# Optimization experiments

Measured on AMD Instinct MI355X. Metric: run time of the kernel, lower is better.

Reference implementation:

```python
import jax, jax.numpy as jnp
import numpy as np

BATCH, SEQ, DIM = 4, 4096, 256
DT_RANK, D_STATE, NUM_TOKENS = 16, 16, 1024


def _adapool(x, T):
    # uniform window mean == AdaptiveAvgPool1d when S % T == 0
    B, S, D = x.shape
    return x.reshape(B, T, S // T, D).mean(axis=2)


def _layernorm(x, g, b, eps=1e-5):
    mu = x.mean(-1, keepdims=True)
    var = ((x - mu) ** 2).mean(-1, keepdims=True)
    return (x - mu) * jax.lax.rsqrt(var + eps) * g + b


def _gauss_mask(T):
    c = (T + 1) // 2
    idx = jnp.arange(T, dtype=jnp.float32)
    sigma = jnp.abs(idx - c).mean()
    w = jnp.exp(-0.5 * (idx - c) ** 2 / sigma ** 2)
    return w / w.sum()


def _ssm(x, Wdbc, Wdt, bdt, Alog, D):
    A = -jnp.exp(Alog)                                     # (Dm, N)
    dbc = x @ Wdbc.T                                       # (B,L,dt+2N)
    delta = jax.nn.softplus(dbc[..., :DT_RANK] @ Wdt.T + bdt)   # (B,L,Dm)
    Bm = dbc[..., DT_RANK:DT_RANK + D_STATE]               # (B,L,N)
    Cm = dbc[..., DT_RANK + D_STATE:]                      # (B,L,N)
    deltaA = jnp.exp(delta[..., None] * A)                 # (B,L,Dm,N)
    BX = (delta[..., None] * Bm[:, :, None, :]) * x[..., None]
    def comb(c1, c2):
        a1, x1 = c1
        a2, x2 = c2
        return (a2 * a1, a2 * x1 + x2)
    _, hs = jax.lax.associative_scan(comb, (deltaA, BX), axis=1)
    y = jnp.einsum('bldn,bln->bld', hs, Cm) + D * x
    return y


def setup_inputs():
    key = jax.random.key(0)
    ks = jax.random.split(key, 16)
    s = 0.05
    Alog = jnp.tile(jnp.log(jnp.arange(1.0, D_STATE + 1.0, dtype=jnp.float32))[None, :], (DIM, 1))
    return {
        'x': jax.random.normal(ks[0], (BATCH, SEQ, DIM), jnp.float32),
        'ln_g': jnp.ones((DIM,), jnp.float32),
        'ln_b': jnp.zeros((DIM,), jnp.float32),
        'W1': jax.random.normal(ks[1], (DIM, DIM), jnp.float32) * s,
        'b1': jnp.zeros((DIM,), jnp.float32),
        'W2': jax.random.normal(ks[2], (DIM, DIM), jnp.float32) * s,
        'b2': jnp.zeros((DIM,), jnp.float32),
        'Wcf': jax.random.normal(ks[3], (DIM, DIM), jnp.float32) * s,
        'bcf': jnp.zeros((DIM,), jnp.float32),
        'Wcb': jax.random.normal(ks[4], (DIM, DIM), jnp.float32) * s,
        'bcb': jnp.zeros((DIM,), jnp.float32),
        'Wdbc_f': jax.random.normal(ks[5], (DT_RANK + 2 * D_STATE, DIM), jnp.float32) * s,
        'Wdt_f': jax.random.normal(ks[6], (DIM, DT_RANK), jnp.float32) * s,
        'bdt_f': jnp.zeros((DIM,), jnp.float32),
        'Alog_f': Alog,
        'D_f': jnp.ones((DIM,), jnp.float32),
        'Wdbc_b': jax.random.normal(ks[7], (DT_RANK + 2 * D_STATE, DIM), jnp.float32) * s,
        'Wdt_b': jax.random.normal(ks[8], (DIM, DT_RANK), jnp.float32) * s,
        'bdt_b': jnp.zeros((DIM,), jnp.float32),
        'Alog_b': Alog,
        'D_b': jnp.ones((DIM,), jnp.float32),
    }


def reference(x, ln_g, ln_b, W1, b1, W2, b2, Wcf, bcf, Wcb, bcb,
              Wdbc_f, Wdt_f, bdt_f, Alog_f, D_f,
              Wdbc_b, Wdt_b, bdt_b, Alog_b, D_b):
    skip = _adapool(x, NUM_TOKENS)
    xn = _layernorm(x, ln_g, ln_b)
    z = xn @ W1.T + b1
    xp = xn @ W2.T + b2
    mask = _gauss_mask(NUM_TOKENS)[None, :, None]

    # forward direction: 1x1 conv (= channel linear) -> softplus -> SSM
    h1 = jax.nn.softplus(jnp.einsum('bsd,ed->bse', xp, Wcf) + bcf)
    x1 = _ssm(h1, Wdbc_f, Wdt_f, bdt_f, Alog_f, D_f)
    x1 = jax.nn.silu(_adapool(x1, NUM_TOKENS) * mask)

    # backward direction on flipped sequence
    h2 = jax.nn.softplus(jnp.einsum('bsd,ed->bse', xp[:, ::-1], Wcb) + bcb)
    x2 = _ssm(h2, Wdbc_b, Wdt_b, bdt_b, Alog_b, D_b)[:, ::-1]
    x2 = jax.nn.silu(_adapool(x2, NUM_TOKENS) * mask)

    zp = jax.nn.silu(_adapool(z, NUM_TOKENS))
    return zp * x1 + zp * x2 + skip
```

## Files before the change

### kernel.cpp

```cpp
#include <hip/hip_runtime.h>
#include <math.h>


namespace {
constexpr int BB = 4;
constexpr int LL = 4096;
constexpr int DD = 256;
constexpr int NS = 16;
constexpr int NCH = 128;
constexpr int CLEN = 32;
constexpr int NG  = CLEN / 8;
constexpr int TOK = 1024;

constexpr size_t NROW = (size_t)BB * LL;
constexpr size_t NE   = NROW * DD;
constexpr size_t NP   = (size_t)BB * TOK * DD;
constexpr size_t NBC  = NROW * NS;
constexpr size_t NAGG = 2ull * BB * DD * NCH * NS;
constexpr size_t NSD  = 2ull * BB * NCH * DD;

constexpr size_t O_H1X  = 0;
constexpr size_t O_G2X  = NE / 2;
constexpr size_t O_H1T  = NE;
constexpr size_t O_G2T  = NE + NE / 2;
constexpr size_t O_DLTF = 2 * NE;
constexpr size_t O_XN   = O_DLTF;
constexpr size_t O_DLTB = 2 * NE + NE / 2;
constexpr size_t O_BMF  = 3 * NE;
constexpr size_t O_CMF  = O_BMF + NBC / 2;
constexpr size_t O_BMB  = O_CMF + NBC / 2;
constexpr size_t O_CMB  = O_BMB + NBC / 2;
constexpr size_t O_ZP   = O_CMB + NBC / 2;
constexpr size_t O_WF1  = O_ZP + NP;
constexpr size_t O_BF1  = O_WF1 + 768 * 256 / 2;
constexpr size_t O_WF2F = O_BF1 + 768;
constexpr size_t O_B2F  = O_WF2F + 384 * 256 / 2;
constexpr size_t O_WF2B = O_B2F + 384;
constexpr size_t O_B2B  = O_WF2B + 384 * 256 / 2;
constexpr size_t O_SD   = O_B2B + 384;
constexpr size_t O_HEND = O_SD + NSD;
constexpr size_t O_HIN  = O_HEND + NAGG / 2;
constexpr size_t O_MASK = O_HIN + NAGG / 2;

constexpr int SST = 136;
}

typedef __bf16 bf16x8 __attribute__((ext_vector_type(8)));
typedef __bf16 bf16x4 __attribute__((ext_vector_type(4)));
typedef float f32x4 __attribute__((ext_vector_type(4)));

__device__ __forceinline__ float softplusf(float x) {
    return fmaxf(x, 0.f) + __logf(1.f + __expf(-fabsf(x)));
}
__device__ __forceinline__ float siluf(float x) {
    return x / (1.f + __expf(-x));
}
__device__ __forceinline__ void gl_lds16(const void* g, void* l) {
    __builtin_amdgcn_global_load_lds((const __attribute__((address_space(1))) unsigned int*)g,
                                     (__attribute__((address_space(3))) unsigned int*)l, 16, 0, 0);
}
__device__ __forceinline__ int st_addr(int col, int row) {
    return col * SST + ((((row >> 3) ^ (col >> 3)) & 15) << 3) + (row & 7);
}
__device__ __forceinline__ void pow_chain(float e1, float* p) {
    p[0] = e1;
    p[1] = e1 * e1;
    p[2] = p[1] * e1;
    p[3] = p[1] * p[1];
    p[4] = p[3] * p[0];
    p[5] = p[3] * p[1];
    p[6] = p[3] * p[2];
    p[7] = p[3] * p[3];
    p[8]  = p[7] * p[0];
    p[9]  = p[7] * p[1];
    p[10] = p[7] * p[2];
    p[11] = p[7] * p[3];
    p[12] = p[7] * p[4];
    p[13] = p[7] * p[5];
    p[14] = p[7] * p[6];
    p[15] = p[7] * p[7];
}

__global__ __launch_bounds__(256) void prep_ln_kernel(
    const float* __restrict__ x, const float* __restrict__ lng, const float* __restrict__ lnb,
    const float* __restrict__ W1, const float* __restrict__ b1,
    const float* __restrict__ W2, const float* __restrict__ b2,
    const float* __restrict__ Wcf, const float* __restrict__ bcf,
    const float* __restrict__ Wcb, const float* __restrict__ bcb,
    const float* __restrict__ Wdt_f, const float* __restrict__ Wdbc_f, const float* __restrict__ bdt_f,
    const float* __restrict__ Wdt_b, const float* __restrict__ Wdbc_b, const float* __restrict__ bdt_b,
    __bf16* __restrict__ xn, float* __restrict__ outp,
    __bf16* __restrict__ Wf1, float* __restrict__ bf1,
    __bf16* __restrict__ Wf2f, float* __restrict__ b2f,
    __bf16* __restrict__ Wf2b, float* __restrict__ b2b,
    float* __restrict__ mask)
{
    int bxg = blockIdx.x;
    int k = threadIdx.x;
    if (bxg < 4096) {
        __shared__ float red[32];
        __shared__ float mv[8];
        int t = k;
        int r0 = bxg * 4;
        float gg = lng[t], bbv = lnb[t];
        float v[4], s[4], q[4];
#pragma unroll
        for (int i = 0; i < 4; ++i) {
            v[i] = x[(size_t)(r0 + i) * 256 + t];
            s[i] = v[i];
            q[i] = v[i] * v[i];
        }
        for (int o = 32; o > 0; o >>= 1) {
#pragma unroll
            for (int i = 0; i < 4; ++i) {
                s[i] += __shfl_xor(s[i], o, 64);
                q[i] += __shfl_xor(q[i], o, 64);
            }
        }
        if ((t & 63) == 0) {
            int w = t >> 6;
#pragma unroll
            for (int i = 0; i < 4; ++i) { red[i * 4 + w] = s[i]; red[16 + i * 4 + w] = q[i]; }
        }
        __syncthreads();
        if (t < 4) {
            float S = red[t * 4 + 0] + red[t * 4 + 1] + red[t * 4 + 2] + red[t * 4 + 3];
            float Q = red[16 + t * 4 + 0] + red[16 + t * 4 + 1] + red[16 + t * 4 + 2] + red[16 + t * 4 + 3];
            float mu = S * (1.f / 256.f);
            mv[t * 2] = mu;
            mv[t * 2 + 1] = rsqrtf(Q * (1.f / 256.f) - mu * mu + 1e-5f);
        }
        __syncthreads();
        float acc = 0.f;
#pragma unroll
        for (int i = 0; i < 4; ++i) {
            xn[(size_t)(r0 + i) * 256 + t] = (__bf16)((v[i] - mv[i * 2]) * mv[i * 2 + 1] * gg + bbv);
            acc += v[i];
        }
        int b = r0 >> 12;
        int g = (r0 & 4095) >> 2;
        outp[((size_t)b * TOK + g) * 256 + t] = acc * 0.25f;
        return;
    }
    int j2 = bxg - 4096;
    int mat = j2 / 641;
    int bx = j2 % 641;
    if (bx < 256) {
        int j = bx;
        const float* Wc = mat ? Wcb : Wcf;
        float acc = 0.f, accb = 0.f;
#pragma unroll 8
        for (int m = 0; m < 256; ++m) {
            float w = Wc[j * 256 + m];
            acc  = fmaf(w, W2[m * 256 + k], acc);
            accb = fmaf(w, b2[m], accb);
        }
        Wf1[(size_t)(256 + mat * 256 + j) * 256 + k] = (__bf16)acc;
        if (k == 0) bf1[256 + mat * 256 + j] = accb + (mat ? bcb[j] : bcf[j]);
        if (mat == 0) {
            Wf1[(size_t)j * 256 + k] = (__bf16)W1[j * 256 + k];
            if (k == 0) bf1[j] = b1[j];
        }
    } else if (bx < 640) {
        int j = bx - 256;
        const float* Wdt  = mat ? Wdt_b : Wdt_f;
        const float* Wdbc = mat ? Wdbc_b : Wdbc_f;
        const float* bdt  = mat ? bdt_b : bdt_f;
        __bf16* Wf2 = mat ? Wf2b : Wf2f;
        float* b2x  = mat ? b2b : b2f;
        float val;
        if (j < 256) {
            float acc = 0.f;
#pragma unroll
            for (int m = 0; m < 16; ++m)
                acc = fmaf(Wdt[j * 16 + m], Wdbc[m * 256 + k], acc);
            val = acc;
        } else if (j < 288) {
            val = Wdbc[(16 + (j - 256)) * 256 + k];
        } else {
            val = 0.f;
        }
        Wf2[(size_t)j * 256 + k] = (__bf16)val;
        if (k == 0) b2x[j] = (j < 256) ? bdt[j] : 0.f;
    } else if (mat == 0) {
        __shared__ float red2[4];
        __shared__ float sb;
        float w[4];
        float loc = 0.f;
#pragma unroll
        for (int q = 0; q < 4; ++q) {
            float dd = (float)(k + 256 * q) - 512.f;
            w[q] = __expf(-0.5f * dd * dd * (1.f / 65536.f));
            loc += w[q];
        }
        for (int o = 32; o > 0; o >>= 1) loc += __shfl_xor(loc, o, 64);
        if ((k & 63) == 0) red2[k >> 6] = loc;
        __syncthreads();
        if (k == 0) sb = red2[0] + red2[1] + red2[2] + red2[3];
        __syncthreads();
        float inv = 1.f / sb;
#pragma unroll
        for (int q = 0; q < 4; ++q) mask[k + 256 * q] = w[q] * inv;
    }
}

__global__ __launch_bounds__(256) void gemm1_mfma(
    const __bf16* __restrict__ A, const __bf16* __restrict__ Bw, const float* __restrict__ bias,
    float* __restrict__ zp, __bf16* __restrict__ h1x, __bf16* __restrict__ g2x,
    __bf16* __restrict__ h1T, __bf16* __restrict__ g2T)
{
    __shared__ __align__(16) __bf16 SH[128 * SST];
    __bf16* As = SH;
    __bf16* Bs = SH + 8192;
    int tid = threadIdx.x;
    int lane = tid & 63, wv = tid >> 6;
    int wr = wv >> 1, wc = wv & 1;
    int lm = lane & 15, lq = lane >> 4;
    int m0 = blockIdx.x << 7, n0 = blockIdx.y << 7;

    const __bf16* gaB = A  + (size_t)(m0 + wv * 32 + lm) * 256 + lq * 8;
    const __bf16* gbB = Bw + (size_t)(n0 + wv * 32 + lm) * 256 + lq * 8;

    f32x4 acc[4][4];
#pragma unroll
    for (int i = 0; i < 4; ++i)
#pragma unroll
        for (int j = 0; j < 4; ++j) acc[i][j] = 0;

    for (int k0 = 0; k0 < 256; k0 += 64) {
        __syncthreads();
#pragma unroll
        for (int rg = 0; rg < 2; ++rg) {
#pragma unroll
            for (int kh = 0; kh < 2; ++kh) {
                gl_lds16(gaB + rg * 16 * 256 + k0 + kh * 32, &As[((wv * 2 + rg) * 2 + kh) * 512]);
                gl_lds16(gbB + rg * 16 * 256 + k0 + kh * 32, &Bs[((wv * 2 + rg) * 2 + kh) * 512]);
            }
        }
        __syncthreads();
#pragma unroll
        for (int kh = 0; kh < 2; ++kh) {
            bf16x8 af[4], bfr[4];
#pragma unroll
            for (int i = 0; i < 4; ++i)
                af[i] = *(const bf16x8*)&As[((wr * 4 + i) * 2 + kh) * 512 + lane * 8];
#pragma unroll
            for (int j = 0; j < 4; ++j)
                bfr[j] = *(const bf16x8*)&Bs[((wc * 4 + j) * 2 + kh) * 512 + lane * 8];
#pragma unroll
            for (int i = 0; i < 4; ++i)
#pragma unroll
                for (int j = 0; j < 4; ++j)
                    acc[i][j] = __builtin_amdgcn_mfma_f32_16x16x32_bf16(af[i], bfr[j], acc[i][j], 0, 0, 0);
        }
    }

    int target = blockIdx.y >> 1;
    int colbase = (blockIdx.y & 1) * 128;
    __syncthreads();
    if (target == 0) {
        float* zs = (float*)SH;
#pragma unroll
        for (int j = 0; j < 4; ++j) {
            int coll = wc * 64 + j * 16 + lm;
            float bv = bias[n0 + coll];
#pragma unroll
            for (int i = 0; i < 4; ++i) {
                int gl = wr * 16 + i * 4 + lq;
                float s = acc[i][j][0] + acc[i][j][1] + acc[i][j][2] + acc[i][j][3];
                zs[gl * 132 + coll] = siluf(0.25f * s + bv);
            }
        }
        __syncthreads();
        int b = m0 >> 12, g0 = (m0 & 4095) >> 2;
        int rl = tid >> 5;
        int c4 = (tid & 31) * 4;
#pragma unroll
        for (int p = 0; p < 4; ++p) {
            int g = p * 8 + rl;
            float4 v = *(float4*)&zs[g * 132 + c4];
            *(float4*)&zp[((size_t)b * TOK + g0 + g) * 256 + colbase + c4] = v;
        }
    } else {
        __bf16* hs = SH;
#pragma unroll
        for (int j = 0; j < 4; ++j) {
            int coll = wc * 64 + j * 16 + lm;
            float bv = bias[n0 + coll];
#pragma unroll
            for (int i = 0; i < 4; ++i) {
                int rl = wr * 64 + i * 16 + lq * 4;
                bf16x4 v4;
#pragma unroll
                for (int r = 0; r < 4; ++r)
                    v4[r] = (__bf16)softplusf(acc[i][j][r] + bv);
                *(bf16x4*)&hs[st_addr(coll, rl)] = v4;
            }
        }
        __syncthreads();
        __bf16* outp = (target == 1) ? h1x : g2x;
        __bf16* outT = (target == 1) ? h1T : g2T;
        {
            int tg = tid >> 4;
#pragma unroll
            for (int it = 0; it < 8; ++it) {
                int dcol = it * 16 + (tid & 15);
                bf16x8 v = *(const bf16x8*)&hs[dcol * SST + (((tg ^ (dcol >> 3)) & 15) << 3)];
                *(bf16x8*)&outT[(((size_t)(m0 >> 3) + tg) * 256 + colbase + dcol) * 8] = v;
            }
        }
        {
            int rl2 = tid >> 4;
            int c8 = (tid & 15) * 8;
#pragma unroll
            for (int p = 0; p < 8; ++p) {
                int row = p * 16 + rl2;
                bf16x8 v;
#pragma unroll
                for (int e = 0; e < 8; ++e) v[e] = hs[st_addr(c8 + e, row)];
                *(bf16x8*)&outp[(size_t)(m0 + row) * 256 + colbase + c8] = v;
            }
        }
    }
}

__global__ __launch_bounds__(256) void gemm2_mfma(
    const __bf16* __restrict__ h1x, const __bf16* __restrict__ g2x,
    const __bf16* __restrict__ Wf, const float* __restrict__ bf2,
    const __bf16* __restrict__ Wb, const float* __restrict__ bb2,
    __bf16* __restrict__ dTf, __bf16* __restrict__ dTb,
    __bf16* __restrict__ BmF, __bf16* __restrict__ CmF,
    __bf16* __restrict__ BmB, __bf16* __restrict__ CmB)
{
    __shared__ __align__(16) __bf16 SH[128 * SST];
    __bf16* As = SH;
    __bf16* Bs = SH + 8192;
    int tid = threadIdx.x;
    int lane = tid & 63, wv = tid >> 6;
    int wr = wv >> 1, wc = wv & 1;
    int lm = lane & 15, lq = lane >> 4;
    int m0 = blockIdx.x << 7, n0 = blockIdx.y << 7;
    int dir = blockIdx.z;
    const __bf16* A    = dir ? g2x : h1x;
    const __bf16* Bw   = dir ? Wb : Wf;
    const float* bias  = dir ? bb2 : bf2;
    __bf16* dT = dir ? dTb : dTf;
    __bf16* Bm = dir ? BmB : BmF;
    __bf16* Cm = dir ? CmB : CmF;

    const __bf16* gaB = A  + (size_t)(m0 + wv * 32 + lm) * 256 + lq * 8;
    const __bf16* gbB = Bw + (size_t)(n0 + wv * 32 + lm) * 256 + lq * 8;

    f32x4 acc[4][4];
#pragma unroll
    for (int i = 0; i < 4; ++i)
#pragma unroll
        for (int j = 0; j < 4; ++j) acc[i][j] = 0;

    for (int k0 = 0; k0 < 256; k0 += 64) {
        __syncthreads();
#pragma unroll
        for (int rg = 0; rg < 2; ++rg) {
#pragma unroll
            for (int kh = 0; kh < 2; ++kh) {
                gl_lds16(gaB + rg * 16 * 256 + k0 + kh * 32, &As[((wv * 2 + rg) * 2 + kh) * 512]);
                gl_lds16(gbB + rg * 16 * 256 + k0 + kh * 32, &Bs[((wv * 2 + rg) * 2 + kh) * 512]);
            }
        }
        __syncthreads();
#pragma unroll
        for (int kh = 0; kh < 2; ++kh) {
            bf16x8 af[4], bfr[4];
#pragma unroll
            for (int i = 0; i < 4; ++i)
                af[i] = *(const bf16x8*)&As[((wr * 4 + i) * 2 + kh) * 512 + lane * 8];
#pragma unroll
            for (int j = 0; j < 4; ++j)
                bfr[j] = *(const bf16x8*)&Bs[((wc * 4 + j) * 2 + kh) * 512 + lane * 8];
#pragma unroll
            for (int i = 0; i < 4; ++i)
#pragma unroll
                for (int j = 0; j < 4; ++j)
                    acc[i][j] = __builtin_amdgcn_mfma_f32_16x16x32_bf16(af[i], bfr[j], acc[i][j], 0, 0, 0);
        }
    }

    __syncthreads();
    if (blockIdx.y < 2) {
        __bf16* hs = SH;
        int colbase = blockIdx.y * 128;
#pragma unroll
        for (int j = 0; j < 4; ++j) {
            int coll = wc * 64 + j * 16 + lm;
            float bv = bias[n0 + coll];
#pragma unroll
            for (int i = 0; i < 4; ++i) {
                int rl = wr * 64 + i * 16 + lq * 4;
                bf16x4 v4;
#pragma unroll
                for (int r = 0; r < 4; ++r)
                    v4[r] = (__bf16)softplusf(acc[i][j][r] + bv);
                *(bf16x4*)&hs[st_addr(coll, rl)] = v4;
            }
        }
        __syncthreads();
        int tg = tid >> 4;
#pragma unroll
        for (int it = 0; it < 8; ++it) {
            int dcol = it * 16 + (tid & 15);
            bf16x8 v = *(const bf16x8*)&hs[dcol * SST + (((tg ^ (dcol >> 3)) & 15) << 3)];
            *(bf16x8*)&dT[(((size_t)(m0 >> 3) + tg) * 256 + colbase + dcol) * 8] = v;
        }
    } else {
        __bf16* bs_ = SH;
        __bf16* cs_ = SH + 128 * 24;
        if (wc == 0) {
#pragma unroll
            for (int j = 0; j < 2; ++j) {
                int coll = j * 16 + lm;
                float bv = bias[n0 + coll];
                __bf16* dst = j ? cs_ : bs_;
#pragma unroll
                for (int i = 0; i < 4; ++i) {
                    int rl = wr * 64 + i * 16 + lq * 4;
#pragma unroll
                    for (int r = 0; r < 4; ++r)
                        dst[(rl + r) * 24 + lm] = (__bf16)(acc[i][j][r] + bv);
                }
            }
        }
        __syncthreads();
        int row = tid >> 1;
        int c8 = (tid & 1) * 8;
        bf16x8 vb = *(bf16x8*)&bs_[row * 24 + c8];
        bf16x8 vc = *(bf16x8*)&cs_[row * 24 + c8];
        *(bf16x8*)&Bm[(size_t)(m0 + row) * 16 + c8] = vb;
        *(bf16x8*)&Cm[(size_t)(m0 + row) * 16 + c8] = vc;
    }
}

__global__ __launch_bounds__(256) void scan1_kernel(
    const __bf16* __restrict__ dTf, const __bf16* __restrict__ dTb,
    const __bf16* __restrict__ xTf, const __bf16* __restrict__ xTb,
    const __bf16* __restrict__ bmf, const __bf16* __restrict__ bmb,
    const float* __restrict__ alogf, const float* __restrict__ alogb,
    float* __restrict__ sdb, __bf16* __restrict__ hend)
{
    int d = threadIdx.x;
    int c = blockIdx.x, b = blockIdx.y, dir = blockIdx.z;
    const __bf16* dT = dir ? dTb : dTf;
    const __bf16* xT = dir ? xTb : xTf;
    const __bf16* Bm = dir ? bmb : bmf;
    const float* Alog = dir ? alogb : alogf;

    float A[16];
    bool intOK = true;
#pragma unroll
    for (int n = 0; n < 16; ++n) {
        A[n] = -__expf(Alog[(size_t)d * 16 + n]);
        intOK = intOK && (fabsf(A[n] + (float)(n + 1)) < 1e-3f);
    }
    float h[16];
#pragma unroll
    for (int n = 0; n < 16; ++n) h[n] = 0.f;
    float sd = 0.f;
    size_t rg0 = (size_t)b * 512 + (size_t)c * NG;
    size_t rowb = (size_t)b * LL + (size_t)c * CLEN;
    if (intOK) {
        for (int g = 0; g < NG; ++g) {
            int gg = dir ? (NG - 1 - g) : g;
            size_t ti = ((rg0 + gg) * 256 + d) * 8;
            bf16x8 dv = *(const bf16x8*)&dT[ti];
            bf16x8 xv8 = *(const bf16x8*)&xT[ti];
#pragma unroll
            for (int ii = 0; ii < 8; ++ii) {
                int i = dir ? (7 - ii) : ii;
                float dlt = (float)dv[i];
                float xv  = (float)xv8[i];
                float common = dlt * xv;
                sd += dlt;
                float p[16];
                pow_chain(__expf(-dlt), p);
                const bf16x8* Bp = (const bf16x8*)&Bm[(rowb + gg * 8 + i) * NS];
                bf16x8 b0 = Bp[0], b1 = Bp[1];
#pragma unroll
                for (int n = 0; n < 8; ++n) {
                    h[n]     = fmaf(p[n],     h[n],     common * (float)b0[n]);
                    h[n + 8] = fmaf(p[n + 8], h[n + 8], common * (float)b1[n]);
                }
            }
        }
    } else {
        for (int g = 0; g < NG; ++g) {
            int gg = dir ? (NG - 1 - g) : g;
            size_t ti = ((rg0 + gg) * 256 + d) * 8;
            bf16x8 dv = *(const bf16x8*)&dT[ti];
            bf16x8 xv8 = *(const bf16x8*)&xT[ti];
#pragma unroll
            for (int ii = 0; ii < 8; ++ii) {
                int i = dir ? (7 - ii) : ii;
                float dlt = (float)dv[i];
                float xv  = (float)xv8[i];
                float common = dlt * xv;
                sd += dlt;
                const bf16x8* Bp = (const bf16x8*)&Bm[(rowb + gg * 8 + i) * NS];
                bf16x8 b0 = Bp[0], b1 = Bp[1];
#pragma unroll
                for (int n = 0; n < 8; ++n) {
                    h[n]     = fmaf(__expf(dlt * A[n]),     h[n],     common * (float)b0[n]);
                    h[n + 8] = fmaf(__expf(dlt * A[n + 8]), h[n + 8], common * (float)b1[n]);
                }
            }
        }
    }
    size_t sbase = (size_t)(dir * 4 + b) * NCH + c;
    sdb[sbase * 256 + d] = sd;
    size_t hb = sbase * 16 * 256 + d;
#pragma unroll
    for (int n = 0; n < 16; ++n) hend[hb + (size_t)n * 256] = (__bf16)h[n];
}

__global__ __launch_bounds__(256) void scan2_kernel(
    const float* __restrict__ sdb, const __bf16* __restrict__ hend,
    const float* __restrict__ alogf, const float* __restrict__ alogb,
    __bf16* __restrict__ hin)
{
    int blk = blockIdx.x;
    int n = blk & 15, b = (blk >> 4) & 3, dir = blk >> 6;
    int d = threadIdx.x;
    const float* Alog = dir ? alogb : alogf;
    float A_dn = -__expf(Alog[(size_t)d * 16 + n]);
    size_t basec = (size_t)(dir * 4 + b) * NCH;
    float s = 0.f;
    if (!dir) {
#pragma unroll 8
        for (int c = 0; c < NCH; ++c) {
            float sdv = sdb[(basec + c) * 256 + d];
            size_t idx = ((basec + c) * 16 + n) * 256 + d;
            float he = (float)hend[idx];
            hin[idx] = (__bf16)s;
            s = fmaf(__expf(sdv * A_dn), s, he);
        }
    } else {
#pragma unroll 8
        for (int c = NCH - 1; c >= 0; --c) {
            float sdv = sdb[(basec + c) * 256 + d];
            size_t idx = ((basec + c) * 16 + n) * 256 + d;
            float he = (float)hend[idx];
            hin[idx] = (__bf16)s;
            s = fmaf(__expf(sdv * A_dn), s, he);
        }
    }
}

__global__ __launch_bounds__(256) void scan3_kernel(
    const __bf16* __restrict__ dTf, const __bf16* __restrict__ dTb,
    const __bf16* __restrict__ xTf, const __bf16* __restrict__ xTb,
    const __bf16* __restrict__ bmf, const __bf16* __restrict__ bmb,
    const __bf16* __restrict__ cmf, const __bf16* __restrict__ cmb,
    const float* __restrict__ alogf, const float* __restrict__ alogb,
    const float* __restrict__ Dfp, const float* __restrict__ Dbp,
    const __bf16* __restrict__ hin,
    const float* __restrict__ zp, const float* __restrict__ mask,
    float* __restrict__ outp)
{
    int d = threadIdx.x;
    int c = blockIdx.x, b = blockIdx.y, dir = blockIdx.z;
    const __bf16* dT = dir ? dTb : dTf;
    const __bf16* xT = dir ? xTb : xTf;
    const __bf16* Bm = dir ? bmb : bmf;
    const __bf16* Cm = dir ? cmb : cmf;
    const float* Alog = dir ? alogb : alogf;
    const float* Dv   = dir ? Dbp : Dfp;

    float A[16];
    bool intOK = true;
#pragma unroll
    for (int n = 0; n < 16; ++n) {
        A[n] = -__expf(Alog[(size_t)d * 16 + n]);
        intOK = intOK && (fabsf(A[n] + (float)(n + 1)) < 1e-3f);
    }
    float Dd = Dv[d];
    float h[16];
    size_t hb = ((size_t)(dir * 4 + b) * NCH + c) * 16 * 256 + d;
#pragma unroll
    for (int n = 0; n < 16; ++n) h[n] = (float)hin[hb + (size_t)n * 256];

    size_t rg0 = (size_t)b * 512 + (size_t)c * NG;
    size_t rowb = (size_t)b * LL + (size_t)c * CLEN;
    int base = c * CLEN;
    float pool = 0.f;
    if (intOK) {
        for (int g = 0; g < NG; ++g) {
            int gg = dir ? (NG - 1 - g) : g;
            size_t ti = ((rg0 + gg) * 256 + d) * 8;
            bf16x8 dv = *(const bf16x8*)&dT[ti];
            bf16x8 xv8 = *(const bf16x8*)&xT[ti];
#pragma unroll
            for (int ii = 0; ii < 8; ++ii) {
                int i = dir ? (7 - ii) : ii;
                float dlt = (float)dv[i];
                float xv  = (float)xv8[i];
                float common = dlt * xv;
                float p[16];
                pow_chain(__expf(-dlt), p);
                size_t row = rowb + gg * 8 + i;
                const bf16x8* Bp = (const bf16x8*)&Bm[row * NS];
                const bf16x8* Cp = (const bf16x8*)&Cm[row * NS];
                bf16x8 b0 = Bp[0], b1 = Bp[1];
                bf16x8 c0 = Cp[0], c1 = Cp[1];
                float yac = 0.f;
#pragma unroll
                for (int n = 0; n < 8; ++n) {
                    h[n]     = fmaf(p[n],     h[n],     common * (float)b0[n]);
                    h[n + 8] = fmaf(p[n + 8], h[n + 8], common * (float)b1[n]);
                    yac = fmaf(h[n], (float)c0[n], yac);
                    yac = fmaf(h[n + 8], (float)c1[n], yac);
                }
                pool += yac + Dd * xv;
                int t = base + gg * 8 + i;
                bool gend = dir ? ((t & 3) == 0) : ((t & 3) == 3);
                if (gend) {
                    int gtok = t >> 2;
                    size_t ip = ((size_t)b * TOK + gtok) * 256 + d;
                    float contrib = zp[ip] * siluf(pool * 0.25f * mask[gtok]);
                    atomicAdd(&outp[ip], contrib);
                    pool = 0.f;
                }
            }
        }
    } else {
        for (int g = 0; g < NG; ++g) {
            int gg = dir ? (NG - 1 - g) : g;
            size_t ti = ((rg0 + gg) * 256 + d) * 8;
            bf16x8 dv = *(const bf16x8*)&dT[ti];
            bf16x8 xv8 = *(const bf16x8*)&xT[ti];
#pragma unroll
            for (int ii = 0; ii < 8; ++ii) {
                int i = dir ? (7 - ii) : ii;
                float dlt = (float)dv[i];
                float xv  = (float)xv8[i];
                float common = dlt * xv;
                size_t row = rowb + gg * 8 + i;
                const bf16x8* Bp = (const bf16x8*)&Bm[row * NS];
                const bf16x8* Cp = (const bf16x8*)&Cm[row * NS];
                bf16x8 b0 = Bp[0], b1 = Bp[1];
                bf16x8 c0 = Cp[0], c1 = Cp[1];
                float yac = 0.f;
#pragma unroll
                for (int n = 0; n < 8; ++n) {
                    h[n]     = fmaf(__expf(dlt * A[n]),     h[n],     common * (float)b0[n]);
                    h[n + 8] = fmaf(__expf(dlt * A[n + 8]), h[n + 8], common * (float)b1[n]);
                    yac = fmaf(h[n], (float)c0[n], yac);
                    yac = fmaf(h[n + 8], (float)c1[n], yac);
                }
                pool += yac + Dd * xv;
                int t = base + gg * 8 + i;
                bool gend = dir ? ((t & 3) == 0) : ((t & 3) == 3);
                if (gend) {
                    int gtok = t >> 2;
                    size_t ip = ((size_t)b * TOK + gtok) * 256 + d;
                    float contrib = zp[ip] * siluf(pool * 0.25f * mask[gtok]);
                    atomicAdd(&outp[ip], contrib);
                    pool = 0.f;
                }
            }
        }
    }
}

extern "C" void kernel_launch(void* const* d_in, const int* in_sizes, int n_in,
                              void* d_out, int out_size, void* d_ws, size_t ws_size,
                              hipStream_t stream)
{
    const float* x      = (const float*)d_in[0];
    const float* ln_g   = (const float*)d_in[1];
    const float* ln_b   = (const float*)d_in[2];
    const float* W1     = (const float*)d_in[3];
    const float* b1     = (const float*)d_in[4];
    const float* W2     = (const float*)d_in[5];
    const float* b2     = (const float*)d_in[6];
    const float* Wcf    = (const float*)d_in[7];
    const float* bcf    = (const float*)d_in[8];
    const float* Wcb    = (const float*)d_in[9];
    const float* bcb    = (const float*)d_in[10];
    const float* Wdbc_f = (const float*)d_in[11];
    const float* Wdt_f  = (const float*)d_in[12];
    const float* bdt_f  = (const float*)d_in[13];
    const float* Alog_f = (const float*)d_in[14];
    const float* D_f    = (const float*)d_in[15];
    const float* Wdbc_b = (const float*)d_in[16];
    const float* Wdt_b  = (const float*)d_in[17];
    const float* bdt_b  = (const float*)d_in[18];
    const float* Alog_b = (const float*)d_in[19];
    const float* D_b    = (const float*)d_in[20];
    float* out = (float*)d_out;
    float* ws  = (float*)d_ws;

    __bf16* h1x = (__bf16*)(ws + O_H1X);
    __bf16* g2x = (__bf16*)(ws + O_G2X);
    __bf16* h1T = (__bf16*)(ws + O_H1T);
    __bf16* g2T = (__bf16*)(ws + O_G2T);
    __bf16* xnb = (__bf16*)(ws + O_XN);
    __bf16* dTf = (__bf16*)(ws + O_DLTF);
    __bf16* dTb = (__bf16*)(ws + O_DLTB);
    __bf16* bmf = (__bf16*)(ws + O_BMF);
    __bf16* cmf = (__bf16*)(ws + O_CMF);
    __bf16* bmb = (__bf16*)(ws + O_BMB);
    __bf16* cmb = (__bf16*)(ws + O_CMB);
    float* zpb  = ws + O_ZP;
    __bf16* wf1 = (__bf16*)(ws + O_WF1);
    float* bf1  = ws + O_BF1;
    __bf16* wf2f = (__bf16*)(ws + O_WF2F);
    float* b2f  = ws + O_B2F;
    __bf16* wf2b = (__bf16*)(ws + O_WF2B);
    float* b2b  = ws + O_B2B;
    float* sdb  = ws + O_SD;
    __bf16* hnd = (__bf16*)(ws + O_HEND);
    __bf16* hin = (__bf16*)(ws + O_HIN);
    float* mkb  = ws + O_MASK;

    prep_ln_kernel<<<dim3(4096 + 1282), 256, 0, stream>>>(
        x, ln_g, ln_b,
        W1, b1, W2, b2, Wcf, bcf, Wcb, bcb,
        Wdt_f, Wdbc_f, bdt_f, Wdt_b, Wdbc_b, bdt_b,
        xnb, out, wf1, bf1, wf2f, b2f, wf2b, b2b, mkb);
    gemm1_mfma<<<dim3(128, 6), 256, 0, stream>>>(xnb, wf1, bf1, zpb, h1x, g2x, h1T, g2T);
    gemm2_mfma<<<dim3(128, 3, 2), 256, 0, stream>>>(h1x, g2x, wf2f, b2f, wf2b, b2b,
                                                    dTf, dTb, bmf, cmf, bmb, cmb);
    scan1_kernel<<<dim3(NCH, BB, 2), 256, 0, stream>>>(dTf, dTb, h1T, g2T, bmf, bmb,
                                                       Alog_f, Alog_b, sdb, hnd);
    scan2_kernel<<<128, 256, 0, stream>>>(sdb, hnd, Alog_f, Alog_b, hin);
    scan3_kernel<<<dim3(NCH, BB, 2), 256, 0, stream>>>(dTf, dTb, h1T, g2T, bmf, bmb, cmf, cmb,
                                                       Alog_f, Alog_b, D_f, D_b, hin,
                                                       zpb, mkb, out);
}
```

Baseline: 218.5 us.

## Pool LayerNorm output before z projection and shrink B/C projection tiles

The LayerNorm kernel now also writes a 4-row mean of the normalized activations, so the z projection (linear, then pooled) runs as a small GEMM over pooled rows instead of over the full sequence. This removes three quarters of that GEMM's work and the later reduction. Separately, the B/C projection in the second GEMM gets its own tile of 256 rows by 32 columns, so it no longer wastes a 128x128 tile on only 32 useful columns. In exchange, gemm1 launches blocks that exit early and writes zp with scattered scalar stores, and the pooled input is rounded to bf16.

Measured after the change: 227.9 us. +4.3%, slower.

```diff
diff --git a/kernel.cpp b/kernel.cpp
--- a/kernel.cpp
+++ b/kernel.cpp
@@ -41,6 +41,7 @@
 constexpr size_t O_HEND = O_SD + NSD;
 constexpr size_t O_HIN  = O_HEND + NAGG / 2;
 constexpr size_t O_MASK = O_HIN + NAGG / 2;
+constexpr size_t O_XNP  = O_MASK + 1024;
 
 constexpr int SST = 136;
 }
@@ -89,7 +90,7 @@
     const float* __restrict__ Wcb, const float* __restrict__ bcb,
     const float* __restrict__ Wdt_f, const float* __restrict__ Wdbc_f, const float* __restrict__ bdt_f,
     const float* __restrict__ Wdt_b, const float* __restrict__ Wdbc_b, const float* __restrict__ bdt_b,
-    __bf16* __restrict__ xn, float* __restrict__ outp,
+    __bf16* __restrict__ xn, __bf16* __restrict__ xnp, float* __restrict__ outp,
     __bf16* __restrict__ Wf1, float* __restrict__ bf1,
     __bf16* __restrict__ Wf2f, float* __restrict__ b2f,
     __bf16* __restrict__ Wf2b, float* __restrict__ b2b,
@@ -131,15 +132,18 @@
             mv[t * 2 + 1] = rsqrtf(Q * (1.f / 256.f) - mu * mu + 1e-5f);
         }
         __syncthreads();
-        float acc = 0.f;
+        float acc = 0.f, lnsum = 0.f;
 #pragma unroll
         for (int i = 0; i < 4; ++i) {
-            xn[(size_t)(r0 + i) * 256 + t] = (__bf16)((v[i] - mv[i * 2]) * mv[i * 2 + 1] * gg + bbv);
+            float lnv = (v[i] - mv[i * 2]) * mv[i * 2 + 1] * gg + bbv;
+            xn[(size_t)(r0 + i) * 256 + t] = (__bf16)lnv;
+            lnsum += lnv;
             acc += v[i];
         }
         int b = r0 >> 12;
         int g = (r0 & 4095) >> 2;
         outp[((size_t)b * TOK + g) * 256 + t] = acc * 0.25f;
+        xnp[(size_t)bxg * 256 + t] = (__bf16)(lnsum * 0.25f);
         return;
     }
     int j2 = bxg - 4096;
@@ -205,7 +209,8 @@
 }
 
 __global__ __launch_bounds__(256) void gemm1_mfma(
-    const __bf16* __restrict__ A, const __bf16* __restrict__ Bw, const float* __restrict__ bias,
+    const __bf16* __restrict__ A, const __bf16* __restrict__ Ap,
+    const __bf16* __restrict__ Bw, const float* __restrict__ bias,
     float* __restrict__ zp, __bf16* __restrict__ h1x, __bf16* __restrict__ g2x,
     __bf16* __restrict__ h1T, __bf16* __restrict__ g2T)
 {
@@ -216,10 +221,23 @@
     int lane = tid & 63, wv = tid >> 6;
     int wr = wv >> 1, wc = wv & 1;
     int lm = lane & 15, lq = lane >> 4;
-    int m0 = blockIdx.x << 7, n0 = blockIdx.y << 7;
-
-    const __bf16* gaB = A  + (size_t)(m0 + wv * 32 + lm) * 256 + lq * 8;
-    const __bf16* gbB = Bw + (size_t)(n0 + wv * 32 + lm) * 256 + lq * 8;
+    int y = blockIdx.y;
+
+    int m0, n0;
+    const __bf16* Arow;
+    if (y == 4) {
+        if (blockIdx.x >= 64) return;
+        m0 = (blockIdx.x >> 1) << 7;
+        n0 = (blockIdx.x & 1) << 7;
+        Arow = Ap;
+    } else {
+        m0 = blockIdx.x << 7;
+        n0 = 256 + y * 128;
+        Arow = A;
+    }
+
+    const __bf16* gaB = Arow + (size_t)(m0 + wv * 32 + lm) * 256 + lq * 8;
+    const __bf16* gbB = Bw   + (size_t)(n0 + wv * 32 + lm) * 256 + lq * 8;
 
     f32x4 acc[4][4];
 #pragma unroll
@@ -255,71 +273,62 @@
         }
     }
 
-    int target = blockIdx.y >> 1;
-    int colbase = (blockIdx.y & 1) * 128;
-    __syncthreads();
-    if (target == 0) {
-        float* zs = (float*)SH;
+    if (y == 4) {
 #pragma unroll
         for (int j = 0; j < 4; ++j) {
             int coll = wc * 64 + j * 16 + lm;
             float bv = bias[n0 + coll];
 #pragma unroll
             for (int i = 0; i < 4; ++i) {
-                int gl = wr * 16 + i * 4 + lq;
-                float s = acc[i][j][0] + acc[i][j][1] + acc[i][j][2] + acc[i][j][3];
-                zs[gl * 132 + coll] = siluf(0.25f * s + bv);
-            }
-        }
-        __syncthreads();
-        int b = m0 >> 12, g0 = (m0 & 4095) >> 2;
-        int rl = tid >> 5;
-        int c4 = (tid & 31) * 4;
-#pragma unroll
-        for (int p = 0; p < 4; ++p) {
-            int g = p * 8 + rl;
-            float4 v = *(float4*)&zs[g * 132 + c4];
-            *(float4*)&zp[((size_t)b * TOK + g0 + g) * 256 + colbase + c4] = v;
-        }
-    } else {
-        __bf16* hs = SH;
-#pragma unroll
-        for (int j = 0; j < 4; ++j) {
-            int coll = wc * 64 + j * 16 + lm;
-            float bv = bias[n0 + coll];
-#pragma unroll
-            for (int i = 0; i < 4; ++i) {
                 int rl = wr * 64 + i * 16 + lq * 4;
-                bf16x4 v4;
 #pragma unroll
                 for (int r = 0; r < 4; ++r)
-                    v4[r] = (__bf16)softplusf(acc[i][j][r] + bv);
-                *(bf16x4*)&hs[st_addr(coll, rl)] = v4;
-            }
-        }
-        __syncthreads();
-        __bf16* outp = (target == 1) ? h1x : g2x;
-        __bf16* outT = (target == 1) ? h1T : g2T;
-        {
-            int tg = tid >> 4;
-#pragma unroll
-            for (int it = 0; it < 8; ++it) {
-                int dcol = it * 16 + (tid & 15);
-                bf16x8 v = *(const bf16x8*)&hs[dcol * SST + (((tg ^ (dcol >> 3)) & 15) << 3)];
-                *(bf16x8*)&outT[(((size_t)(m0 >> 3) + tg) * 256 + colbase + dcol) * 8] = v;
-            }
-        }
-        {
-            int rl2 = tid >> 4;
-            int c8 = (tid & 15) * 8;
-#pragma unroll
-            for (int p = 0; p < 8; ++p) {
-                int row = p * 16 + rl2;
-                bf16x8 v;
-#pragma unroll
-                for (int e = 0; e < 8; ++e) v[e] = hs[st_addr(c8 + e, row)];
-                *(bf16x8*)&outp[(size_t)(m0 + row) * 256 + colbase + c8] = v;
-            }
+                    zp[(size_t)(m0 + rl + r) * 256 + n0 + coll] = siluf(acc[i][j][r] + bv);
+            }
+        }
+        return;
+    }
+
+    int target = 1 + (y >> 1);
+    int colbase = (y & 1) * 128;
+    __syncthreads();
+    __bf16* hs = SH;
+#pragma unroll
+    for (int j = 0; j < 4; ++j) {
+        int coll = wc * 64 + j * 16 + lm;
+        float bv = bias[n0 + coll];
+#pragma unroll
+        for (int i = 0; i < 4; ++i) {
+            int rl = wr * 64 + i * 16 + lq * 4;
+            bf16x4 v4;
+#pragma unroll
+            for (int r = 0; r < 4; ++r)
+                v4[r] = (__bf16)softplusf(acc[i][j][r] + bv);
+            *(bf16x4*)&hs[st_addr(coll, rl)] = v4;
+        }
+    }
+    __syncthreads();
+    __bf16* outp = (target == 1) ? h1x : g2x;
+    __bf16* outT = (target == 1) ? h1T : g2T;
+    {
+        int tg = tid >> 4;
+#pragma unroll
+        for (int it = 0; it < 8; ++it) {
+            int dcol = it * 16 + (tid & 15);
+            bf16x8 v = *(const bf16x8*)&hs[dcol * SST + (((tg ^ (dcol >> 3)) & 15) << 3)];
+            *(bf16x8*)&outT[(((size_t)(m0 >> 3) + tg) * 256 + colbase + dcol) * 8] = v;
+        }
+    }
+    {
+        int rl2 = tid >> 4;
+        int c8 = (tid & 15) * 8;
+#pragma unroll
+        for (int p = 0; p < 8; ++p) {
+            int row = p * 16 + rl2;
+            bf16x8 v;
+#pragma unroll
+            for (int e = 0; e < 8; ++e) v[e] = hs[st_addr(c8 + e, row)];
+            *(bf16x8*)&outp[(size_t)(m0 + row) * 256 + colbase + c8] = v;
         }
     }
 }
@@ -332,14 +341,10 @@
     __bf16* __restrict__ BmF, __bf16* __restrict__ CmF,
     __bf16* __restrict__ BmB, __bf16* __restrict__ CmB)
 {
-    __shared__ __align__(16) __bf16 SH[128 * SST];
-    __bf16* As = SH;
-    __bf16* Bs = SH + 8192;
+    __shared__ __align__(16) __bf16 SH[18432];
     int tid = threadIdx.x;
     int lane = tid & 63, wv = tid >> 6;
-    int wr = wv >> 1, wc = wv & 1;
     int lm = lane & 15, lq = lane >> 4;
-    int m0 = blockIdx.x << 7, n0 = blockIdx.y << 7;
     int dir = blockIdx.z;
     const __bf16* A    = dir ? g2x : h1x;
     const __bf16* Bw   = dir ? Wb : Wf;
@@ -348,6 +353,89 @@
     __bf16* Bm = dir ? BmB : BmF;
     __bf16* Cm = dir ? CmB : CmF;
 
+    if (blockIdx.y == 2) {
+        if (blockIdx.x >= 64) return;
+        __bf16* As = SH;
+        __bf16* Bs = SH + 16384;
+        int m0 = blockIdx.x << 8;
+        const __bf16* gaB = A  + (size_t)(m0 + wv * 64 + lm) * 256 + lq * 8;
+        const __bf16* gbB = Bw + (size_t)(256 + lm) * 256 + lq * 8;
+
+        f32x4 acc[4][2];
+#pragma unroll
+        for (int i = 0; i < 4; ++i)
+#pragma unroll
+            for (int j = 0; j < 2; ++j) acc[i][j] = 0;
+
+        for (int k0 = 0; k0 < 256; k0 += 64) {
+            __syncthreads();
+#pragma unroll
+            for (int rg = 0; rg < 4; ++rg) {
+#pragma unroll
+                for (int kh = 0; kh < 2; ++kh) {
+                    gl_lds16(gaB + rg * 16 * 256 + k0 + kh * 32, &As[((wv * 4 + rg) * 2 + kh) * 512]);
+                }
+            }
+            if (wv == 0) {
+#pragma unroll
+                for (int rg = 0; rg < 2; ++rg) {
+#pragma unroll
+                    for (int kh = 0; kh < 2; ++kh) {
+                        gl_lds16(gbB + rg * 16 * 256 + k0 + kh * 32, &Bs[(rg * 2 + kh) * 512]);
+                    }
+                }
+            }
+            __syncthreads();
+#pragma unroll
+            for (int kh = 0; kh < 2; ++kh) {
+                bf16x8 af[4], bfr[2];
+#pragma unroll
+                for (int i = 0; i < 4; ++i)
+                    af[i] = *(const bf16x8*)&As[((wv * 4 + i) * 2 + kh) * 512 + lane * 8];
+#pragma unroll
+                for (int j = 0; j < 2; ++j)
+                    bfr[j] = *(const bf16x8*)&Bs[(j * 2 + kh) * 512 + lane * 8];
+#pragma unroll
+                for (int i = 0; i < 4; ++i)
+#pragma unroll
+                    for (int j = 0; j < 2; ++j)
+                        acc[i][j] = __builtin_amdgcn_mfma_f32_16x16x32_bf16(af[i], bfr[j], acc[i][j], 0, 0, 0);
+            }
+        }
+
+        __syncthreads();
+        __bf16* bs_ = SH;
+        __bf16* cs_ = SH + 256 * 24;
+#pragma unroll
+        for (int j = 0; j < 2; ++j) {
+            float bv = bias[256 + j * 16 + lm];
+            __bf16* dst = j ? cs_ : bs_;
+#pragma unroll
+            for (int i = 0; i < 4; ++i) {
+                int rl = wv * 64 + i * 16 + lq * 4;
+#pragma unroll
+                for (int r = 0; r < 4; ++r)
+                    dst[(rl + r) * 24 + lm] = (__bf16)(acc[i][j][r] + bv);
+            }
+        }
+        __syncthreads();
+#pragma unroll
+        for (int p = 0; p < 2; ++p) {
+            int row = p * 128 + (tid >> 1);
+            int c8 = (tid & 1) * 8;
+            bf16x8 vb = *(bf16x8*)&bs_[row * 24 + c8];
+            bf16x8 vc = *(bf16x8*)&cs_[row * 24 + c8];
+            *(bf16x8*)&Bm[(size_t)(m0 + row) * 16 + c8] = vb;
+            *(bf16x8*)&Cm[(size_t)(m0 + row) * 16 + c8] = vc;
+        }
+        return;
+    }
+
+    __bf16* As = SH;
+    __bf16* Bs = SH + 8192;
+    int wr = wv >> 1, wc = wv & 1;
+    int m0 = blockIdx.x << 7, n0 = blockIdx.y << 7;
+
     const __bf16* gaB = A  + (size_t)(m0 + wv * 32 + lm) * 256 + lq * 8;
     const __bf16* gbB = Bw + (size_t)(n0 + wv * 32 + lm) * 256 + lq * 8;
 
@@ -386,56 +474,29 @@
     }
 
     __syncthreads();
-    if (blockIdx.y < 2) {
-        __bf16* hs = SH;
-        int colbase = blockIdx.y * 128;
-#pragma unroll
-        for (int j = 0; j < 4; ++j) {
-            int coll = wc * 64 + j * 16 + lm;
-            float bv = bias[n0 + coll];
-#pragma unroll
-            for (int i = 0; i < 4; ++i) {
-                int rl = wr * 64 + i * 16 + lq * 4;
-                bf16x4 v4;
-#pragma unroll
-                for (int r = 0; r < 4; ++r)
-                    v4[r] = (__bf16)softplusf(acc[i][j][r] + bv);
-                *(bf16x4*)&hs[st_addr(coll, rl)] = v4;
-            }
-        }
-        __syncthreads();
-        int tg = tid >> 4;
-#pragma unroll
-        for (int it = 0; it < 8; ++it) {
-            int dcol = it * 16 + (tid & 15);
-            bf16x8 v = *(const bf16x8*)&hs[dcol * SST + (((tg ^ (dcol >> 3)) & 15) << 3)];
-            *(bf16x8*)&dT[(((size_t)(m0 >> 3) + tg) * 256 + colbase + dcol) * 8] = v;
-        }
-    } else {
-        __bf16* bs_ = SH;
-        __bf16* cs_ = SH + 128 * 24;
-        if (wc == 0) {
-#pragma unroll
-            for (int j = 0; j < 2; ++j) {
-                int coll = j * 16 + lm;
-                float bv = bias[n0 + coll];
-                __bf16* dst = j ? cs_ : bs_;
-#pragma unroll
-                for (int i = 0; i < 4; ++i) {
-                    int rl = wr * 64 + i * 16 + lq * 4;
-#pragma unroll
-                    for (int r = 0; r < 4; ++r)
-                        dst[(rl + r) * 24 + lm] = (__bf16)(acc[i][j][r] + bv);
-                }
-            }
-        }
-        __syncthreads();
-        int row = tid >> 1;
-        int c8 = (tid & 1) * 8;
-        bf16x8 vb = *(bf16x8*)&bs_[row * 24 + c8];
-        bf16x8 vc = *(bf16x8*)&cs_[row * 24 + c8];
-        *(bf16x8*)&Bm[(size_t)(m0 + row) * 16 + c8] = vb;
-        *(bf16x8*)&Cm[(size_t)(m0 + row) * 16 + c8] = vc;
+    __bf16* hs = SH;
+    int colbase = blockIdx.y * 128;
+#pragma unroll
+    for (int j = 0; j < 4; ++j) {
+        int coll = wc * 64 + j * 16 + lm;
+        float bv = bias[n0 + coll];
+#pragma unroll
+        for (int i = 0; i < 4; ++i) {
+            int rl = wr * 64 + i * 16 + lq * 4;
+            bf16x4 v4;
+#pragma unroll
+            for (int r = 0; r < 4; ++r)
+                v4[r] = (__bf16)softplusf(acc[i][j][r] + bv);
+            *(bf16x4*)&hs[st_addr(coll, rl)] = v4;
+        }
+    }
+    __syncthreads();
+    int tg = tid >> 4;
+#pragma unroll
+    for (int it = 0; it < 8; ++it) {
+        int dcol = it * 16 + (tid & 15);
+        bf16x8 v = *(const bf16x8*)&hs[dcol * SST + (((tg ^ (dcol >> 3)) & 15) << 3)];
+        *(bf16x8*)&dT[(((size_t)(m0 >> 3) + tg) * 256 + colbase + dcol) * 8] = v;
     }
 }
 
@@ -719,13 +780,14 @@
     __bf16* hnd = (__bf16*)(ws + O_HEND);
     __bf16* hin = (__bf16*)(ws + O_HIN);
     float* mkb  = ws + O_MASK;
+    __bf16* xnp = (__bf16*)(ws + O_XNP);
 
     prep_ln_kernel<<<dim3(4096 + 1282), 256, 0, stream>>>(
         x, ln_g, ln_b,
         W1, b1, W2, b2, Wcf, bcf, Wcb, bcb,
         Wdt_f, Wdbc_f, bdt_f, Wdt_b, Wdbc_b, bdt_b,
-        xnb, out, wf1, bf1, wf2f, b2f, wf2b, b2b, mkb);
-    gemm1_mfma<<<dim3(128, 6), 256, 0, stream>>>(xnb, wf1, bf1, zpb, h1x, g2x, h1T, g2T);
+        xnb, xnp, out, wf1, bf1, wf2f, b2f, wf2b, b2b, mkb);
+    gemm1_mfma<<<dim3(128, 5), 256, 0, stream>>>(xnb, xnp, wf1, bf1, zpb, h1x, g2x, h1T, g2T);
     gemm2_mfma<<<dim3(128, 3, 2), 256, 0, stream>>>(h1x, g2x, wf2f, b2f, wf2b, b2b,
                                                     dTf, dTb, bmf, cmf, bmb, cmb);
     scan1_kernel<<<dim3(NCH, BB, 2), 256, 0, stream>>>(dTf, dTb, h1T, g2T, bmf, bmb,
```

## Double-buffer GEMM K-loop with async LDS loads and split scan2 blocks

Applied to the files above, without the earlier changes.

Both MFMA GEMM kernels replace the single-buffered 64-wide K loop with a double-buffered 32-wide K loop. The next K slice's global-to-LDS loads are issued before computing on the current slice, with explicit vmcnt waits and barriers, so memory latency overlaps MFMA work. scan2 is relaunched as 256 blocks of 128 threads instead of 128 blocks of 256, spreading the serial chunk scan over more CUs. The pipelined loop depends on hand-placed waitcnt and barrier ordering, which is fragile.

Result: faster. 213.1 us (-2.5%).

```diff
diff --git a/kernel.cpp b/kernel.cpp
--- a/kernel.cpp
+++ b/kernel.cpp
@@ -80,6 +80,47 @@
     p[14] = p[7] * p[6];
     p[15] = p[7] * p[7];
 }
+
+#define GEMM_KLOOP(SHBASE, GA, GB, WR, WC, WV, LANE, ACC)                          \
+    {                                                                               \
+        _Pragma("unroll")                                                           \
+        for (int rg = 0; rg < 2; ++rg) {                                            \
+            gl_lds16((GA) + rg * 16 * 256, &(SHBASE)[((WV) * 2 + rg) * 512]);       \
+            gl_lds16((GB) + rg * 16 * 256, &(SHBASE)[4096 + ((WV) * 2 + rg) * 512]);\
+        }                                                                           \
+        _Pragma("unroll")                                                           \
+        for (int kst = 0; kst < 8; ++kst) {                                         \
+            if (kst < 7) {                                                          \
+                __bf16* Asn = (SHBASE) + ((kst + 1) & 1) * 8192;                    \
+                int k0n = (kst + 1) * 32;                                           \
+                _Pragma("unroll")                                                   \
+                for (int rg = 0; rg < 2; ++rg) {                                    \
+                    gl_lds16((GA) + rg * 16 * 256 + k0n, &Asn[((WV) * 2 + rg) * 512]);      \
+                    gl_lds16((GB) + rg * 16 * 256 + k0n, &Asn[4096 + ((WV) * 2 + rg) * 512]);\
+                }                                                                   \
+                asm volatile("s_waitcnt vmcnt(4)" ::: "memory");                    \
+            } else {                                                                \
+                asm volatile("s_waitcnt vmcnt(0)" ::: "memory");                    \
+            }                                                                       \
+            __builtin_amdgcn_s_barrier();                                           \
+            __builtin_amdgcn_sched_barrier(0);                                      \
+            const __bf16* Ac = (SHBASE) + (kst & 1) * 8192;                         \
+            const __bf16* Bc = Ac + 4096;                                           \
+            bf16x8 af[4], bfr[4];                                                   \
+            _Pragma("unroll")                                                       \
+            for (int i = 0; i < 4; ++i)                                             \
+                af[i] = *(const bf16x8*)&Ac[((WR) * 4 + i) * 512 + (LANE) * 8];     \
+            _Pragma("unroll")                                                       \
+            for (int j = 0; j < 4; ++j)                                             \
+                bfr[j] = *(const bf16x8*)&Bc[((WC) * 4 + j) * 512 + (LANE) * 8];    \
+            _Pragma("unroll")                                                       \
+            for (int i = 0; i < 4; ++i)                                             \
+                _Pragma("unroll")                                                   \
+                for (int j = 0; j < 4; ++j)                                         \
+                    ACC[i][j] = __builtin_amdgcn_mfma_f32_16x16x32_bf16(af[i], bfr[j], ACC[i][j], 0, 0, 0); \
+            __builtin_amdgcn_s_barrier();                                           \
+        }                                                                           \
+    }
 
 __global__ __launch_bounds__(256) void prep_ln_kernel(
     const float* __restrict__ x, const float* __restrict__ lng, const float* __restrict__ lnb,
@@ -210,8 +251,6 @@
     __bf16* __restrict__ h1T, __bf16* __restrict__ g2T)
 {
     __shared__ __align__(16) __bf16 SH[128 * SST];
-    __bf16* As = SH;
-    __bf16* Bs = SH + 8192;
     int tid = threadIdx.x;
     int lane = tid & 63, wv = tid >> 6;
     int wr = wv >> 1, wc = wv & 1;
@@ -227,33 +266,7 @@
 #pragma unroll
         for (int j = 0; j < 4; ++j) acc[i][j] = 0;
 
-    for (int k0 = 0; k0 < 256; k0 += 64) {
-        __syncthreads();
-#pragma unroll
-        for (int rg = 0; rg < 2; ++rg) {
-#pragma unroll
-            for (int kh = 0; kh < 2; ++kh) {
-                gl_lds16(gaB + rg * 16 * 256 + k0 + kh * 32, &As[((wv * 2 + rg) * 2 + kh) * 512]);
-                gl_lds16(gbB + rg * 16 * 256 + k0 + kh * 32, &Bs[((wv * 2 + rg) * 2 + kh) * 512]);
-            }
-        }
-        __syncthreads();
-#pragma unroll
-        for (int kh = 0; kh < 2; ++kh) {
-            bf16x8 af[4], bfr[4];
-#pragma unroll
-            for (int i = 0; i < 4; ++i)
-                af[i] = *(const bf16x8*)&As[((wr * 4 + i) * 2 + kh) * 512 + lane * 8];
-#pragma unroll
-            for (int j = 0; j < 4; ++j)
-                bfr[j] = *(const bf16x8*)&Bs[((wc * 4 + j) * 2 + kh) * 512 + lane * 8];
-#pragma unroll
-            for (int i = 0; i < 4; ++i)
-#pragma unroll
-                for (int j = 0; j < 4; ++j)
-                    acc[i][j] = __builtin_amdgcn_mfma_f32_16x16x32_bf16(af[i], bfr[j], acc[i][j], 0, 0, 0);
-        }
-    }
+    GEMM_KLOOP(SH, gaB, gbB, wr, wc, wv, lane, acc)
 
     int target = blockIdx.y >> 1;
     int colbase = (blockIdx.y & 1) * 128;
@@ -333,8 +346,6 @@
     __bf16* __restrict__ BmB, __bf16* __restrict__ CmB)
 {
     __shared__ __align__(16) __bf16 SH[128 * SST];
-    __bf16* As = SH;
-    __bf16* Bs = SH + 8192;
     int tid = threadIdx.x;
     int lane = tid & 63, wv = tid >> 6;
     int wr = wv >> 1, wc = wv & 1;
@@ -357,33 +368,7 @@
 #pragma unroll
         for (int j = 0; j < 4; ++j) acc[i][j] = 0;
 
-    for (int k0 = 0; k0 < 256; k0 += 64) {
-        __syncthreads();
-#pragma unroll
-        for (int rg = 0; rg < 2; ++rg) {
-#pragma unroll
-            for (int kh = 0; kh < 2; ++kh) {
-                gl_lds16(gaB + rg * 16 * 256 + k0 + kh * 32, &As[((wv * 2 + rg) * 2 + kh) * 512]);
-                gl_lds16(gbB + rg * 16 * 256 + k0 + kh * 32, &Bs[((wv * 2 + rg) * 2 + kh) * 512]);
-            }
-        }
-        __syncthreads();
-#pragma unroll
-        for (int kh = 0; kh < 2; ++kh) {
-            bf16x8 af[4], bfr[4];
-#pragma unroll
-            for (int i = 0; i < 4; ++i)
-                af[i] = *(const bf16x8*)&As[((wr * 4 + i) * 2 + kh) * 512 + lane * 8];
-#pragma unroll
-            for (int j = 0; j < 4; ++j)
-                bfr[j] = *(const bf16x8*)&Bs[((wc * 4 + j) * 2 + kh) * 512 + lane * 8];
-#pragma unroll
-            for (int i = 0; i < 4; ++i)
-#pragma unroll
-                for (int j = 0; j < 4; ++j)
-                    acc[i][j] = __builtin_amdgcn_mfma_f32_16x16x32_bf16(af[i], bfr[j], acc[i][j], 0, 0, 0);
-        }
-    }
+    GEMM_KLOOP(SH, gaB, gbB, wr, wc, wv, lane, acc)
 
     __syncthreads();
     if (blockIdx.y < 2) {
@@ -520,14 +505,14 @@
     for (int n = 0; n < 16; ++n) hend[hb + (size_t)n * 256] = (__bf16)h[n];
 }
 
-__global__ __launch_bounds__(256) void scan2_kernel(
+__global__ __launch_bounds__(128) void scan2_kernel(
     const float* __restrict__ sdb, const __bf16* __restrict__ hend,
     const float* __restrict__ alogf, const float* __restrict__ alogb,
     __bf16* __restrict__ hin)
 {
-    int blk = blockIdx.x;
+    int blk = blockIdx.x >> 1;
     int n = blk & 15, b = (blk >> 4) & 3, dir = blk >> 6;
-    int d = threadIdx.x;
+    int d = ((blockIdx.x & 1) << 7) + threadIdx.x;
     const float* Alog = dir ? alogb : alogf;
     float A_dn = -__expf(Alog[(size_t)d * 16 + n]);
     size_t basec = (size_t)(dir * 4 + b) * NCH;
@@ -730,7 +715,7 @@
                                                     dTf, dTb, bmf, cmf, bmb, cmb);
     scan1_kernel<<<dim3(NCH, BB, 2), 256, 0, stream>>>(dTf, dTb, h1T, g2T, bmf, bmb,
                                                        Alog_f, Alog_b, sdb, hnd);
-    scan2_kernel<<<128, 256, 0, stream>>>(sdb, hnd, Alog_f, Alog_b, hin);
+    scan2_kernel<<<256, 128, 0, stream>>>(sdb, hnd, Alog_f, Alog_b, hin);
     scan3_kernel<<<dim3(NCH, BB, 2), 256, 0, stream>>>(dTf, dTb, h1T, g2T, bmf, bmb, cmf, cmb,
                                                        Alog_f, Alog_b, D_f, D_b, hin,
                                                        zpb, mkb, out);
```
